# Optimization experiments

Measured on AMD Instinct MI355X. Metric: run time of the kernel, lower is better.

Reference implementation:

```python
import jax, jax.numpy as jnp
import numpy as np

EPS = 1.0  # epsilon in fix_box_coordinates

def _fix_box_coordinates(boxes):
    x1 = jnp.minimum(boxes[..., 0], boxes[..., 2])
    y1 = jnp.minimum(boxes[..., 1], boxes[..., 3])
    x2 = jnp.maximum(boxes[..., 0], boxes[..., 2])
    y2 = jnp.maximum(boxes[..., 1], boxes[..., 3])
    x2 = jnp.maximum(x2, x1 + EPS)
    y2 = jnp.maximum(y2, y1 + EPS)
    return jnp.stack([x1, y1, x2, y2], axis=-1)

def _box_iou(boxes1, boxes2):
    # torchvision.ops.box_iou: pairwise IoU [N, M]
    area1 = (boxes1[:, 2] - boxes1[:, 0]) * (boxes1[:, 3] - boxes1[:, 1])  # [N]
    area2 = (boxes2[:, 2] - boxes2[:, 0]) * (boxes2[:, 3] - boxes2[:, 1])  # [M]
    lt = jnp.maximum(boxes1[:, None, :2], boxes2[None, :, :2])  # [N, M, 2]
    rb = jnp.minimum(boxes1[:, None, 2:], boxes2[None, :, 2:])  # [N, M, 2]
    wh = jnp.clip(rb - lt, 0.0, None)                            # [N, M, 2]
    inter = wh[..., 0] * wh[..., 1]                              # [N, M]
    union = area1[:, None] + area2[None, :] - inter
    return inter / union

def setup_inputs() -> dict:
    key = jax.random.key(0)
    k1, k2 = jax.random.split(key)
    N, M = 8192, 8192
    pred_boxes = jax.random.uniform(k1, (N, 4), dtype=jnp.float32)
    true_boxes = jax.random.uniform(k2, (M, 4), dtype=jnp.float32)
    return {"pred_boxes": pred_boxes, "true_boxes": true_boxes}

def reference(pred_boxes, true_boxes):
    pred = _fix_box_coordinates(pred_boxes.reshape(-1, 4))
    true = _fix_box_coordinates(true_boxes.reshape(-1, 4))
    iou_matrix = _box_iou(pred, true)          # [N, M]
    max_iou = jnp.max(iou_matrix, axis=0)      # [M]
    return 1.0 - max_iou
```

## Files before the change

### kernel.cpp

```cpp
#include <hip/hip_runtime.h>

#define BLOCK 256
#define TPB 4
#define CHUNK 128
#define WAVES (BLOCK / 64)

__global__ void init_out(float* __restrict__ out, int M) {
    int i = blockIdx.x * blockDim.x + threadIdx.x;
    if (i < M) out[i] = 1.0f;
}

__global__ __launch_bounds__(BLOCK) void iou_fused(
    const float* __restrict__ pred,
    const float* __restrict__ trub,
    float* __restrict__ out,
    int N, int M)
{
    __shared__ float2 sp[CHUNK];
    __shared__ float4 sbox[CHUNK];
    __shared__ float  sarea[CHUNK];
    __shared__ int    sbadw[WAVES];

    const int tid = threadIdx.x;
    const int n0  = blockIdx.y * CHUNK;

    bool bad = false;
    if (tid < CHUNK) {
        int k = n0 + tid; if (k >= N) k = N - 1;
        float4 b = reinterpret_cast<const float4*>(pred)[k];
        float x1 = fminf(b.x, b.z), y1 = fminf(b.y, b.w);
        float x2 = fmaxf(b.x, b.z), y2 = fmaxf(b.y, b.w);
        bad = (x2 > x1 + 1.0f) || (y2 > y1 + 1.0f);
        x2 = fmaxf(x2, x1 + 1.0f); y2 = fmaxf(y2, y1 + 1.0f);
        sp[tid]    = make_float2(x1, y1);
        sbox[tid]  = make_float4(x1, y1, x2, y2);
        sarea[tid] = (x2 - x1) * (y2 - y1);
    }

    const int jbase = blockIdx.x * (BLOCK * TPB) + tid;
    float tx[TPB], ty[TPB], X2[TPB], Y2[TPB], TA[TPB];
#pragma unroll
    for (int t = 0; t < TPB; ++t) {
        int j = jbase + t * BLOCK; if (j >= M) j = M - 1;
        float4 b = reinterpret_cast<const float4*>(trub)[j];
        float x1 = fminf(b.x, b.z), y1 = fminf(b.y, b.w);
        float x2 = fmaxf(b.x, b.z), y2 = fmaxf(b.y, b.w);
        bad = bad || (x2 > x1 + 1.0f) || (y2 > y1 + 1.0f);
        x2 = fmaxf(x2, x1 + 1.0f); y2 = fmaxf(y2, y1 + 1.0f);
        tx[t] = x1; ty[t] = y1; X2[t] = x2; Y2[t] = y2;
        TA[t] = (x2 - x1) * (y2 - y1);
    }

    int anybad = __any(bad) ? 1 : 0;
    if ((tid & 63) == 0) sbadw[tid >> 6] = anybad;
    __syncthreads();
    int blkbad = 0;
#pragma unroll
    for (int w = 0; w < WAVES; ++w) blkbad |= sbadw[w];

    float best[TPB];
#pragma unroll
    for (int t = 0; t < TPB; ++t) best[t] = 0.0f;

    if (!blkbad) {
#pragma unroll
        for (int k = 0; k < CHUNK; ++k) {
            float2 p = sp[k];
#pragma unroll
            for (int t = 0; t < TPB; ++t) {
                float wx = 1.0f - fabsf(p.x - tx[t]);
                float hy = fmaxf(1.0f - fabsf(p.y - ty[t]), 0.0f);
                best[t] = fmaxf(best[t], wx * hy);
            }
        }
#pragma unroll
        for (int t = 0; t < TPB; ++t)
            best[t] = best[t] * __builtin_amdgcn_rcpf(2.0f - best[t]);
    } else {
#pragma unroll 4
        for (int k = 0; k < CHUNK; ++k) {
            float4 p  = sbox[k];
            float  pa = sarea[k];
#pragma unroll
            for (int t = 0; t < TPB; ++t) {
                float lx = fmaxf(p.x, tx[t]);
                float ly = fmaxf(p.y, ty[t]);
                float rx = fminf(p.z, X2[t]);
                float ry = fminf(p.w, Y2[t]);
                float w  = fmaxf(rx - lx, 0.0f);
                float h  = fmaxf(ry - ly, 0.0f);
                float inter = w * h;
                float uni   = (pa + TA[t]) - inter;
                best[t] = fmaxf(best[t], inter * __builtin_amdgcn_rcpf(uni));
            }
        }
    }

#pragma unroll
    for (int t = 0; t < TPB; ++t) {
        int j = jbase + t * BLOCK;
        if (j < M) {
            float loss = 1.0f - best[t];
            atomicMin(reinterpret_cast<int*>(out) + j, __float_as_int(loss));
        }
    }
}

extern "C" void kernel_launch(void* const* d_in, const int* in_sizes, int n_in,
                              void* d_out, int out_size, void* d_ws, size_t ws_size,
                              hipStream_t stream) {
    const float* pred = (const float*)d_in[0];
    const float* trub = (const float*)d_in[1];
    float* out = (float*)d_out;
    const int N = in_sizes[0] / 4;
    const int M = in_sizes[1] / 4;

    init_out<<<(M + BLOCK - 1) / BLOCK, BLOCK, 0, stream>>>(out, M);

    dim3 grid((M + BLOCK * TPB - 1) / (BLOCK * TPB),
              (N + CHUNK - 1) / CHUNK);
    iou_fused<<<grid, BLOCK, 0, stream>>>(pred, trub, out, N, M);
}
```

Measured before the change: 19.20 us.

## Replace atomic 2D grid with one-pass per-column block reduction over all preds

Each block now owns a small set of target columns and streams all predicted boxes from global memory, reducing the max IoU with wave shuffles and shared memory instead of global atomicMin. This removes the separate init kernel launch and the atomics. In exchange every block rereads the full pred array through the cache hierarchy rather than sharing a chunk via LDS.

```diff
diff --git a/kernel.cpp b/kernel.cpp
--- a/kernel.cpp
+++ b/kernel.cpp
@@ -1,108 +1,107 @@
 #include <hip/hip_runtime.h>
 
 #define BLOCK 256
-#define TPB 4
-#define CHUNK 128
+#define COLS 8
 #define WAVES (BLOCK / 64)
 
-__global__ void init_out(float* __restrict__ out, int M) {
-    int i = blockIdx.x * blockDim.x + threadIdx.x;
-    if (i < M) out[i] = 1.0f;
-}
-
-__global__ __launch_bounds__(BLOCK) void iou_fused(
+__global__ __launch_bounds__(BLOCK) void iou_onepass(
     const float* __restrict__ pred,
     const float* __restrict__ trub,
     float* __restrict__ out,
     int N, int M)
 {
-    __shared__ float2 sp[CHUNK];
-    __shared__ float4 sbox[CHUNK];
-    __shared__ float  sarea[CHUNK];
-    __shared__ int    sbadw[WAVES];
+    __shared__ float swv[WAVES][COLS];
+    __shared__ int   sbad[WAVES];
 
-    const int tid = threadIdx.x;
-    const int n0  = blockIdx.y * CHUNK;
+    const int tid  = threadIdx.x;
+    const int lane = tid & 63;
+    const int wv   = tid >> 6;
+    const int jb   = blockIdx.x * COLS;
 
+    float tx[COLS], ty[COLS], gx2[COLS], gy2[COLS], ga[COLS];
     bool bad = false;
-    if (tid < CHUNK) {
-        int k = n0 + tid; if (k >= N) k = N - 1;
-        float4 b = reinterpret_cast<const float4*>(pred)[k];
-        float x1 = fminf(b.x, b.z), y1 = fminf(b.y, b.w);
-        float x2 = fmaxf(b.x, b.z), y2 = fmaxf(b.y, b.w);
-        bad = (x2 > x1 + 1.0f) || (y2 > y1 + 1.0f);
-        x2 = fmaxf(x2, x1 + 1.0f); y2 = fmaxf(y2, y1 + 1.0f);
-        sp[tid]    = make_float2(x1, y1);
-        sbox[tid]  = make_float4(x1, y1, x2, y2);
-        sarea[tid] = (x2 - x1) * (y2 - y1);
-    }
-
-    const int jbase = blockIdx.x * (BLOCK * TPB) + tid;
-    float tx[TPB], ty[TPB], X2[TPB], Y2[TPB], TA[TPB];
 #pragma unroll
-    for (int t = 0; t < TPB; ++t) {
-        int j = jbase + t * BLOCK; if (j >= M) j = M - 1;
+    for (int c = 0; c < COLS; ++c) {
+        int j = jb + c; if (j >= M) j = M - 1;
         float4 b = reinterpret_cast<const float4*>(trub)[j];
         float x1 = fminf(b.x, b.z), y1 = fminf(b.y, b.w);
         float x2 = fmaxf(b.x, b.z), y2 = fmaxf(b.y, b.w);
         bad = bad || (x2 > x1 + 1.0f) || (y2 > y1 + 1.0f);
         x2 = fmaxf(x2, x1 + 1.0f); y2 = fmaxf(y2, y1 + 1.0f);
-        tx[t] = x1; ty[t] = y1; X2[t] = x2; Y2[t] = y2;
-        TA[t] = (x2 - x1) * (y2 - y1);
+        tx[c] = x1; ty[c] = y1; gx2[c] = x2; gy2[c] = y2;
+        ga[c] = (x2 - x1) * (y2 - y1);
     }
 
-    int anybad = __any(bad) ? 1 : 0;
-    if ((tid & 63) == 0) sbadw[tid >> 6] = anybad;
+    float best[COLS];
+#pragma unroll
+    for (int c = 0; c < COLS; ++c) best[c] = 0.0f;
+
+#pragma unroll 4
+    for (int i = tid; i < N; i += BLOCK) {
+        float4 b = reinterpret_cast<const float4*>(pred)[i];
+        float x1 = fminf(b.x, b.z), y1 = fminf(b.y, b.w);
+        float x2 = fmaxf(b.x, b.z), y2 = fmaxf(b.y, b.w);
+        bad = bad || (x2 > x1 + 1.0f) || (y2 > y1 + 1.0f);
+#pragma unroll
+        for (int c = 0; c < COLS; ++c) {
+            float wx = 1.0f - fabsf(x1 - tx[c]);
+            float hy = fmaxf(1.0f - fabsf(y1 - ty[c]), 0.0f);
+            best[c] = fmaxf(best[c], wx * hy);
+        }
+    }
+
+    int ab = __any(bad) ? 1 : 0;
+    if (lane == 0) sbad[wv] = ab;
     __syncthreads();
     int blkbad = 0;
 #pragma unroll
-    for (int w = 0; w < WAVES; ++w) blkbad |= sbadw[w];
+    for (int w = 0; w < WAVES; ++w) blkbad |= sbad[w];
 
-    float best[TPB];
+    if (blkbad) {
 #pragma unroll
-    for (int t = 0; t < TPB; ++t) best[t] = 0.0f;
-
-    if (!blkbad) {
+        for (int c = 0; c < COLS; ++c) best[c] = 0.0f;
+        for (int i = tid; i < N; i += BLOCK) {
+            float4 b = reinterpret_cast<const float4*>(pred)[i];
+            float x1 = fminf(b.x, b.z), y1 = fminf(b.y, b.w);
+            float x2 = fmaxf(b.x, b.z), y2 = fmaxf(b.y, b.w);
+            x2 = fmaxf(x2, x1 + 1.0f); y2 = fmaxf(y2, y1 + 1.0f);
+            float pa = (x2 - x1) * (y2 - y1);
 #pragma unroll
-        for (int k = 0; k < CHUNK; ++k) {
-            float2 p = sp[k];
-#pragma unroll
-            for (int t = 0; t < TPB; ++t) {
-                float wx = 1.0f - fabsf(p.x - tx[t]);
-                float hy = fmaxf(1.0f - fabsf(p.y - ty[t]), 0.0f);
-                best[t] = fmaxf(best[t], wx * hy);
-            }
-        }
-#pragma unroll
-        for (int t = 0; t < TPB; ++t)
-            best[t] = best[t] * __builtin_amdgcn_rcpf(2.0f - best[t]);
-    } else {
-#pragma unroll 4
-        for (int k = 0; k < CHUNK; ++k) {
-            float4 p  = sbox[k];
-            float  pa = sarea[k];
-#pragma unroll
-            for (int t = 0; t < TPB; ++t) {
-                float lx = fmaxf(p.x, tx[t]);
-                float ly = fmaxf(p.y, ty[t]);
-                float rx = fminf(p.z, X2[t]);
-                float ry = fminf(p.w, Y2[t]);
+            for (int c = 0; c < COLS; ++c) {
+                float lx = fmaxf(x1, tx[c]);
+                float ly = fmaxf(y1, ty[c]);
+                float rx = fminf(x2, gx2[c]);
+                float ry = fminf(y2, gy2[c]);
                 float w  = fmaxf(rx - lx, 0.0f);
                 float h  = fmaxf(ry - ly, 0.0f);
                 float inter = w * h;
-                float uni   = (pa + TA[t]) - inter;
-                best[t] = fmaxf(best[t], inter * __builtin_amdgcn_rcpf(uni));
+                float uni   = (pa + ga[c]) - inter;
+                best[c] = fmaxf(best[c], inter * __builtin_amdgcn_rcpf(uni));
             }
         }
+    } else {
+#pragma unroll
+        for (int c = 0; c < COLS; ++c)
+            best[c] = best[c] * __builtin_amdgcn_rcpf(2.0f - best[c]);
     }
 
 #pragma unroll
-    for (int t = 0; t < TPB; ++t) {
-        int j = jbase + t * BLOCK;
-        if (j < M) {
-            float loss = 1.0f - best[t];
-            atomicMin(reinterpret_cast<int*>(out) + j, __float_as_int(loss));
-        }
+    for (int c = 0; c < COLS; ++c) {
+#pragma unroll
+        for (int off = 32; off >= 1; off >>= 1)
+            best[c] = fmaxf(best[c], __shfl_xor(best[c], off, 64));
+    }
+    if (lane == 0) {
+#pragma unroll
+        for (int c = 0; c < COLS; ++c) swv[wv][c] = best[c];
+    }
+    __syncthreads();
+    if (tid < COLS) {
+        float m = swv[0][tid];
+#pragma unroll
+        for (int w = 1; w < WAVES; ++w) m = fmaxf(m, swv[w][tid]);
+        int j = jb + tid;
+        if (j < M) out[j] = 1.0f - m;
     }
 }
 
@@ -115,9 +114,6 @@
     const int N = in_sizes[0] / 4;
     const int M = in_sizes[1] / 4;
 
-    init_out<<<(M + BLOCK - 1) / BLOCK, BLOCK, 0, stream>>>(out, M);
-
-    dim3 grid((M + BLOCK * TPB - 1) / (BLOCK * TPB),
-              (N + CHUNK - 1) / CHUNK);
-    iou_fused<<<grid, BLOCK, 0, stream>>>(pred, trub, out, N, M);
+    int nblk = (M + COLS - 1) / COLS;
+    iou_onepass<<<nblk, BLOCK, 0, stream>>>(pred, trub, out, N, M);
 }
```

Result: no change. 19.43 us (+1.2%).
